# Kernel tuning notes

Hardware: AMD Instinct MI355X
Metric: run time of the kernel (lower is better)

## Reference

```python
import jax, jax.numpy as jnp
import numpy as np
from jax import lax

B, L = 4, 1024
D_MODEL = 512
D_INNER = 2 * D_MODEL            # expand=2 -> 1024
HEADDIM = 64
NHEADS = D_INNER // HEADDIM      # 16
D_STATE = 64
D_CONV = 4
NLAYERS = 2
NTOKEN = 60695
PAD_IDX = 60694
NCLS = 164
CONV_DIM = D_INNER + 2 * D_STATE            # 1152 (ngroups=1)
D_IN_PROJ = 2 * D_INNER + 2 * D_STATE + NHEADS  # 2192
MAX_VALUE = 512.0
EPS = 1e-5


def _ln(x, g=None, b=None):
    m = jnp.mean(x, -1, keepdims=True)
    v = jnp.mean((x - m) ** 2, -1, keepdims=True)
    y = (x - m) * lax.rsqrt(v + EPS)
    return y if g is None else y * g + b


def _smart_flip(X, pad_mask):
    # reverse only the valid (non-pad) prefix of each sequence
    lengths = (~pad_mask).sum(1)
    rng = jnp.arange(X.shape[1])[None, :]
    flip = rng < lengths[:, None]
    pos = jnp.where(flip, lengths[:, None] - 1 - rng, rng)
    return jnp.take_along_axis(X, pos[:, :, None], axis=1)


def _mamba2(u, in_w, conv_w, conv_b, A_log, dt_bias, Dskip, norm_w, out_w):
    # Mamba2 block (mamba_ssm defaults: ngroups=1, silu conv act, gated RMSNorm)
    Bb, Ll, _ = u.shape
    zxbcdt = u @ in_w.T                                      # (B,L,D_IN_PROJ)
    z = zxbcdt[..., :D_INNER]
    xBC = zxbcdt[..., D_INNER:D_INNER + CONV_DIM]
    dt = jax.nn.softplus(zxbcdt[..., -NHEADS:] + dt_bias)    # (B,L,H)
    # causal depthwise conv1d + silu
    xBC = jnp.pad(xBC, ((0, 0), (D_CONV - 1, 0), (0, 0))).transpose(0, 2, 1)
    xBC = lax.conv_general_dilated(xBC, conv_w[:, None, :], (1,), 'VALID',
                                   feature_group_count=CONV_DIM)
    xBC = jax.nn.silu(xBC.transpose(0, 2, 1) + conv_b)       # (B,L,CONV_DIM)
    x = xBC[..., :D_INNER].reshape(Bb, Ll, NHEADS, HEADDIM)
    Bm = xBC[..., D_INNER:D_INNER + D_STATE]                 # (B,L,N)
    Cm = xBC[..., D_INNER + D_STATE:]                        # (B,L,N)
    dA = jnp.exp(dt * (-jnp.exp(A_log)))                     # (B,L,H)

    def step(h, t):
        dA_t, dt_t, x_t, B_t, C_t = t
        # h: (B,H,P,N)
        h = h * dA_t[:, :, None, None] \
            + (dt_t[:, :, None] * x_t)[..., None] * B_t[:, None, None, :]
        y = jnp.einsum('bhpn,bn->bhp', h, C_t)
        return h, y

    h0 = jnp.zeros((Bb, NHEADS, HEADDIM, D_STATE), u.dtype)
    xs = (dA.transpose(1, 0, 2), dt.transpose(1, 0, 2),
          x.transpose(1, 0, 2, 3), Bm.transpose(1, 0, 2), Cm.transpose(1, 0, 2))
    _, ys = lax.scan(step, h0, xs)                            # (L,B,H,P)
    y = ys.transpose(1, 0, 2, 3) + Dskip[None, None, :, None] * x
    y = y.reshape(Bb, Ll, D_INNER)
    y = y * jax.nn.silu(z)                                    # gated RMSNorm
    y = y * lax.rsqrt(jnp.mean(y * y, -1, keepdims=True) + EPS) * norm_w
    return y @ out_w.T


def _forward(src, values, pad_mask, embed, ge_ln_g, ge_ln_b,
             ve_w1, ve_b1, ve_w2, ve_b2, ve_ln_g, ve_ln_b,
             in_proj_w, conv_w_f, conv_b_f, A_log_f, dt_bias_f, D_f, norm_w_f,
             conv_w_r, conv_b_r, A_log_r, dt_bias_r, D_r, norm_w_r, out_proj_w,
             expr_w1, expr_b1, expr_w2, expr_b2, expr_w3, expr_b3,
             cls_w1, cls_b1, cls_ln1_g, cls_ln1_b, cls_w2, cls_b2,
             cls_ln2_g, cls_ln2_b, cls_wo, cls_bo):
    src_emb = _ln(embed[src], ge_ln_g, ge_ln_b)
    v = jnp.minimum(values, MAX_VALUE)[..., None]
    v = jax.nn.relu(v @ ve_w1.T + ve_b1)
    v = _ln(v @ ve_w2.T + ve_b2, ve_ln_g, ve_ln_b)
    h = (src_emb + v) * (~pad_mask)[..., None]
    for i in range(NLAYERS):
        hn = _ln(h)  # F.layer_norm without affine
        out = _mamba2(hn, in_proj_w[i], conv_w_f[i], conv_b_f[i], A_log_f[i],
                      dt_bias_f[i], D_f[i], norm_w_f[i], out_proj_w[i])
        rev = _smart_flip(hn, pad_mask)
        out_r = _mamba2(rev, in_proj_w[i], conv_w_r[i], conv_b_r[i], A_log_r[i],
                        dt_bias_r[i], D_r[i], norm_w_r[i], out_proj_w[i])
        out_r = _smart_flip(out_r, pad_mask)
        h = _ln((out + out_r) / 2)
    # ExprDecoder (MLM head)
    e = jax.nn.leaky_relu(h @ expr_w1.T + expr_b1)
    e = jax.nn.leaky_relu(e @ expr_w2.T + expr_b2)
    mlm = (e @ expr_w3.T + expr_b3)[..., 0]
    # cell embedding: cls token
    cell = h[:, 0, :]
    # ClsDecoder
    c = _ln(jax.nn.relu(cell @ cls_w1.T + cls_b1), cls_ln1_g, cls_ln1_b)
    c = _ln(jax.nn.relu(c @ cls_w2.T + cls_b2), cls_ln2_g, cls_ln2_b)
    cls = c @ cls_wo.T + cls_bo
    return mlm, cell, cls


def setup_inputs() -> dict:
    key = jax.random.key(0)
    ks = iter(jax.random.split(key, 64))
    w = lambda *s: jax.random.normal(next(ks), s, jnp.float32) * 0.02
    embed = w(NTOKEN, D_MODEL).at[PAD_IDX].set(0.0)
    dt_u = jax.random.uniform(next(ks), (NLAYERS, NHEADS), minval=1e-3, maxval=0.1)
    dt_u2 = jax.random.uniform(next(ks), (NLAYERS, NHEADS), minval=1e-3, maxval=0.1)
    return dict(
        src=jax.random.randint(next(ks), (B, L), 0, PAD_IDX),
        values=jax.random.uniform(next(ks), (B, L), jnp.float32),
        src_key_padding_mask=jnp.zeros((B, L), bool),
        embed=embed,
        ge_ln_g=jnp.ones((D_MODEL,)), ge_ln_b=jnp.zeros((D_MODEL,)),
        ve_w1=w(D_MODEL, 1), ve_b1=jnp.zeros((D_MODEL,)),
        ve_w2=w(D_MODEL, D_MODEL), ve_b2=jnp.zeros((D_MODEL,)),
        ve_ln_g=jnp.ones((D_MODEL,)), ve_ln_b=jnp.zeros((D_MODEL,)),
        in_proj_w=w(NLAYERS, D_IN_PROJ, D_MODEL),
        conv_w_f=w(NLAYERS, CONV_DIM, D_CONV), conv_b_f=jnp.zeros((NLAYERS, CONV_DIM)),
        A_log_f=jnp.log(jax.random.uniform(next(ks), (NLAYERS, NHEADS), minval=1.0, maxval=16.0)),
        dt_bias_f=dt_u + jnp.log(-jnp.expm1(-dt_u)),
        D_f=jnp.ones((NLAYERS, NHEADS)), norm_w_f=jnp.ones((NLAYERS, D_INNER)),
        conv_w_r=w(NLAYERS, CONV_DIM, D_CONV), conv_b_r=jnp.zeros((NLAYERS, CONV_DIM)),
        A_log_r=jnp.log(jax.random.uniform(next(ks), (NLAYERS, NHEADS), minval=1.0, maxval=16.0)),
        dt_bias_r=dt_u2 + jnp.log(-jnp.expm1(-dt_u2)),
        D_r=jnp.ones((NLAYERS, NHEADS)), norm_w_r=jnp.ones((NLAYERS, D_INNER)),
        out_proj_w=w(NLAYERS, D_MODEL, D_INNER),
        expr_w1=w(D_MODEL, D_MODEL), expr_b1=jnp.zeros((D_MODEL,)),
        expr_w2=w(D_MODEL, D_MODEL), expr_b2=jnp.zeros((D_MODEL,)),
        expr_w3=w(1, D_MODEL), expr_b3=jnp.zeros((1,)),
        cls_w1=w(D_MODEL, D_MODEL), cls_b1=jnp.zeros((D_MODEL,)),
        cls_ln1_g=jnp.ones((D_MODEL,)), cls_ln1_b=jnp.zeros((D_MODEL,)),
        cls_w2=w(D_MODEL, D_MODEL), cls_b2=jnp.zeros((D_MODEL,)),
        cls_ln2_g=jnp.ones((D_MODEL,)), cls_ln2_b=jnp.zeros((D_MODEL,)),
        cls_wo=w(NCLS, D_MODEL), cls_bo=jnp.zeros((NCLS,)),
    )


def reference(src, values, src_key_padding_mask, embed, ge_ln_g, ge_ln_b,
              ve_w1, ve_b1, ve_w2, ve_b2, ve_ln_g, ve_ln_b,
              in_proj_w, conv_w_f, conv_b_f, A_log_f, dt_bias_f, D_f, norm_w_f,
              conv_w_r, conv_b_r, A_log_r, dt_bias_r, D_r, norm_w_r, out_proj_w,
              expr_w1, expr_b1, expr_w2, expr_b2, expr_w3, expr_b3,
              cls_w1, cls_b1, cls_ln1_g, cls_ln1_b, cls_w2, cls_b2,
              cls_ln2_g, cls_ln2_b, cls_wo, cls_bo):
    return _forward(src, values, src_key_padding_mask, embed, ge_ln_g, ge_ln_b,
                    ve_w1, ve_b1, ve_w2, ve_b2, ve_ln_g, ve_ln_b,
                    in_proj_w, conv_w_f, conv_b_f, A_log_f, dt_bias_f, D_f, norm_w_f,
                    conv_w_r, conv_b_r, A_log_r, dt_bias_r, D_r, norm_w_r, out_proj_w,
                    expr_w1, expr_b1, expr_w2, expr_b2, expr_w3, expr_b3,
                    cls_w1, cls_b1, cls_ln1_g, cls_ln1_b, cls_w2, cls_b2,
                    cls_ln2_g, cls_ln2_b, cls_wo, cls_bo)
```

## Files before the change

kernel.cpp:

```cpp
#include <hip/hip_runtime.h>
#include <hip/hip_bf16.h>
#include <math.h>

constexpr int Bb = 4, Ls = 1024, DM = 512, DI = 1024, NH = 16, HD = 64, DS = 64;
constexpr int CDIM = DI + 2 * DS;
constexpr int DIP  = 2 * DI + 2 * DS + NH;
constexpr int NPJ  = 2 * DI + 2 * DS;
constexpr float EPSf = 1e-5f;
constexpr int TOK = Bb * Ls;
constexpr int CH = 64, NCH = Ls / CH;

#define DEVI __device__ __forceinline__

using bfrag = __attribute__((ext_vector_type(8))) short;
using f4v   = __attribute__((ext_vector_type(4))) float;
using u16x8 = __attribute__((ext_vector_type(8))) unsigned short;

#define GLOAD16(gp, lp)                                                              \
  __builtin_amdgcn_global_load_lds((__attribute__((address_space(1))) void*)(gp),   \
                                   (__attribute__((address_space(3))) void*)(lp),   \
                                   16, 0, 0)

DEVI float wsum(float v) {
#pragma unroll
  for (int o = 32; o > 0; o >>= 1) v += __shfl_xor(v, o);
  return v;
}
DEVI float sigmoidf_(float x) { return 1.f / (1.f + __expf(-x)); }
DEVI unsigned short f2bf(float x) {
  union { float f; unsigned u; } c{x};
  unsigned u = c.u;
  u += 0x7fffu + ((u >> 16) & 1u);
  return (unsigned short)(u >> 16);
}
DEVI float bf2f(unsigned short u) {
  union { unsigned u; float f; } c{(unsigned)u << 16};
  return c.f;
}

DEVI void ld8(const float* __restrict__ p, int lane, float (&x)[8]) {
  float4 a = *(const float4*)(p + lane * 4);
  float4 b = *(const float4*)(p + 256 + lane * 4);
  x[0] = a.x; x[1] = a.y; x[2] = a.z; x[3] = a.w;
  x[4] = b.x; x[5] = b.y; x[6] = b.z; x[7] = b.w;
}
DEVI void ld8bf(const unsigned short* __restrict__ p, int lane, float (&x)[8]) {
  ushort4 a = *(const ushort4*)(p + lane * 4);
  ushort4 b = *(const ushort4*)(p + 256 + lane * 4);
  x[0] = bf2f(a.x); x[1] = bf2f(a.y); x[2] = bf2f(a.z); x[3] = bf2f(a.w);
  x[4] = bf2f(b.x); x[5] = bf2f(b.y); x[6] = bf2f(b.z); x[7] = bf2f(b.w);
}
DEVI void st8(float* __restrict__ p, int lane, const float (&x)[8]) {
  *(float4*)(p + lane * 4) = make_float4(x[0], x[1], x[2], x[3]);
  *(float4*)(p + 256 + lane * 4) = make_float4(x[4], x[5], x[6], x[7]);
}
DEVI void st8bf(unsigned short* __restrict__ p, int lane, const float (&x)[8]) {
  *(ushort4*)(p + lane * 4) = make_ushort4(f2bf(x[0]), f2bf(x[1]), f2bf(x[2]), f2bf(x[3]));
  *(ushort4*)(p + 256 + lane * 4) = make_ushort4(f2bf(x[4]), f2bf(x[5]), f2bf(x[6]), f2bf(x[7]));
}
DEVI void norm8(float (&x)[8]) {
  float s = 0;
#pragma unroll
  for (int j = 0; j < 8; ++j) s += x[j];
  float mean = wsum(s) * (1.f / 512.f);
#pragma unroll
  for (int j = 0; j < 8; ++j) x[j] -= mean;
  float q = 0;
#pragma unroll
  for (int j = 0; j < 8; ++j) q += x[j] * x[j];
  float var = wsum(q) * (1.f / 512.f);
  float inv = rsqrtf(var + EPSf);
#pragma unroll
  for (int j = 0; j < 8; ++j) x[j] *= inv;
}

__global__ __launch_bounds__(256) void k_w2bf(const float* __restrict__ in,
                                              unsigned short* __restrict__ out, int n8) {
  int i = blockIdx.x * 256 + threadIdx.x;
  if (i >= n8) return;
  const float4* p = (const float4*)in + (size_t)i * 2;
  float4 a = p[0], b = p[1];
  *((ushort4*)out + (size_t)i * 2) = make_ushort4(f2bf(a.x), f2bf(a.y), f2bf(a.z), f2bf(a.w));
  *((ushort4*)out + (size_t)i * 2 + 1) = make_ushort4(f2bf(b.x), f2bf(b.y), f2bf(b.z), f2bf(b.w));
}

__global__ __launch_bounds__(256) void k_embed(const int* __restrict__ src, const float* __restrict__ values,
    const float* __restrict__ embed, const float* __restrict__ gg, const float* __restrict__ gb,
    const float* __restrict__ vw1, const float* __restrict__ vb1,
    float* __restrict__ hbuf, unsigned short* __restrict__ v1bf) {
  int gw = (blockIdx.x * 256 + threadIdx.x) >> 6;
  int lane = threadIdx.x & 63;
  if (gw >= TOK) return;
  const float* er = embed + (size_t)src[gw] * DM;
  float x[8];
  ld8(er, lane, x);
  norm8(x);
  float g[8], bv[8];
  ld8(gg, lane, g); ld8(gb, lane, bv);
#pragma unroll
  for (int j = 0; j < 8; ++j) x[j] = x[j] * g[j] + bv[j];
  st8(hbuf + (size_t)gw * DM, lane, x);
  float val = fminf(values[gw], 512.f);
  float w1[8], b1[8];
  ld8(vw1, lane, w1); ld8(vb1, lane, b1);
  float v[8];
#pragma unroll
  for (int j = 0; j < 8; ++j) v[j] = fmaxf(val * w1[j] + b1[j], 0.f);
  st8bf(v1bf + (size_t)gw * DM, lane, v);
}

__global__ __launch_bounds__(256) void k_haddv(const float* __restrict__ t2, const float* __restrict__ g,
    const float* __restrict__ bb, const unsigned char* __restrict__ mask, float* __restrict__ hbuf) {
  int gw = (blockIdx.x * 256 + threadIdx.x) >> 6;
  int lane = threadIdx.x & 63;
  if (gw >= TOK) return;
  float x[8];
  ld8(t2 + (size_t)gw * DM, lane, x);
  norm8(x);
  float gv[8], bv[8], h[8];
  ld8(g, lane, gv); ld8(bb, lane, bv);
  ld8(hbuf + (size_t)gw * DM, lane, h);
  float mf = mask[gw] ? 0.f : 1.f;
#pragma unroll
  for (int j = 0; j < 8; ++j) h[j] = (h[j] + x[j] * gv[j] + bv[j]) * mf;
  st8(hbuf + (size_t)gw * DM, lane, h);
}

__global__ __launch_bounds__(256) void k_lndt(const float* __restrict__ pre, const float* __restrict__ inw,
    const float* __restrict__ dtbF, const float* __restrict__ AlogF,
    const float* __restrict__ dtbR, const float* __restrict__ AlogR,
    const int* __restrict__ len, unsigned short* __restrict__ hnbf,
    float* __restrict__ dtf, float* __restrict__ laf,
    float* __restrict__ dtr, float* __restrict__ lar) {
  int gw = (blockIdx.x * 256 + threadIdx.x) >> 6;
  int lane = threadIdx.x & 63;
  if (gw >= TOK) return;
  float x[8];
  ld8(pre + (size_t)gw * DM, lane, x);
  norm8(x);
  st8bf(hnbf + (size_t)gw * DM, lane, x);
  const float* wdt = inw + (size_t)NPJ * DM;
  float myraw = 0.f;
#pragma unroll
  for (int hh = 0; hh < NH; ++hh) {
    float w[8];
    ld8(wdt + (size_t)hh * DM, lane, w);
    float s = 0;
#pragma unroll
    for (int j = 0; j < 8; ++j) s += x[j] * w[j];
    s = wsum(s);
    if (lane == hh) myraw = s;
  }
  if (lane < NH) {
    int t = gw & (Ls - 1), b = gw >> 10;
    int ln = len[b];
    int pos = (t < ln) ? (ln - 1 - t) : t;
    size_t grev = (size_t)(b * Ls + pos);
    float rf = myraw + dtbF[lane];
    float df = rf > 20.f ? rf : log1pf(__expf(rf));
    dtf[(size_t)gw * NH + lane] = df;
    laf[(size_t)gw * NH + lane] = -__expf(AlogF[lane]) * df;
    float rr = myraw + dtbR[lane];
    float dr = rr > 20.f ? rr : log1pf(__expf(rr));
    dtr[grev * NH + lane] = dr;
    lar[grev * NH + lane] = -__expf(AlogR[lane]) * dr;
  }
}

template <int ACT, int OMODE>
__global__ __launch_bounds__(256) void gemm_bf(const unsigned short* __restrict__ A,
    const unsigned short* __restrict__ W, const float* __restrict__ bias,
    void* __restrict__ Cout, int M, int N, int K) {
  constexpr int BK = 64;
  __shared__ unsigned short As[128 * BK];
  __shared__ unsigned short Bs[128 * BK];
  int tid = threadIdx.x;
  int bm = blockIdx.y * 128, bn = blockIdx.x * 128;
  int wv = tid >> 6, lane = tid & 63;
  int mb = (wv >> 1) * 64, nb = (wv & 1) * 64;
  int rA = lane >> 3;
  int cswz = (lane & 7) ^ rA;
  f4v acc[4][4] = {};

  for (int k0 = 0; k0 < K; k0 += BK) {
#pragma unroll
    for (int q = 0; q < 4; ++q) {
      int ch = wv * 4 + q;
      const unsigned short* ga = A + (size_t)(bm + ch * 8 + rA) * K + k0 + cswz * 8;
      GLOAD16(ga, &As[ch * 512]);
      const unsigned short* gb = W + (size_t)(bn + ch * 8 + rA) * K + k0 + cswz * 8;
      GLOAD16(gb, &Bs[ch * 512]);
    }
    __syncthreads();
#pragma unroll
    for (int ks = 0; ks < BK; ks += 32) {
      int kb = (ks >> 3) + (lane >> 4);
      bfrag af[4], bg[4];
#pragma unroll
      for (int i = 0; i < 4; ++i) {
        int ra_ = mb + i * 16 + (lane & 15);
        af[i] = *(const bfrag*)((const char*)As + ((ra_ * 128 + kb * 16) ^ ((ra_ & 7) << 4)));
        int rb_ = nb + i * 16 + (lane & 15);
        bg[i] = *(const bfrag*)((const char*)Bs + ((rb_ * 128 + kb * 16) ^ ((rb_ & 7) << 4)));
      }
#pragma unroll
      for (int i = 0; i < 4; ++i)
#pragma unroll
        for (int j = 0; j < 4; ++j)
          acc[i][j] = __builtin_amdgcn_mfma_f32_16x16x32_bf16(af[i], bg[j], acc[i][j], 0, 0, 0);
    }
    __syncthreads();
  }

  int cb = bn + nb + (lane & 15);
  int rb = bm + mb + ((lane >> 4) << 2);
#pragma unroll
  for (int j = 0; j < 4; ++j) {
    float bv = bias ? bias[cb + j * 16] : 0.f;
#pragma unroll
    for (int i = 0; i < 4; ++i) {
#pragma unroll
      for (int r = 0; r < 4; ++r) {
        float v = acc[i][j][r] + bv;
        if (ACT == 1) v = fmaxf(v, 0.f);
        if (ACT == 2) v = v > 0.f ? v : 0.01f * v;
        size_t idx = (size_t)(rb + i * 16 + r) * N + cb + j * 16;
        if (OMODE == 0) ((float*)Cout)[idx] = v;
        else ((unsigned short*)Cout)[idx] = f2bf(v);
      }
    }
  }
}

__global__ __launch_bounds__(256) void k_convbc(const unsigned short* __restrict__ zx,
    const float* __restrict__ cwF, const float* __restrict__ cbF,
    const float* __restrict__ cwR, const float* __restrict__ cbR,
    const int* __restrict__ len, unsigned short* __restrict__ bcbuf) {
  int idx = blockIdx.x * 256 + threadIdx.x;
  if (idx >= 2 * TOK * 128) return;
  int col = idx & 127;
  int bt = (idx >> 7) & (TOK - 1);
  int dir = idx >> 19;
  int b = bt >> 10, t = bt & (Ls - 1);
  int ln = len[b];
  const float* cw = dir ? cwR : cwF;
  const float* cb = dir ? cbR : cbF;
  int ccd = DI + col;
  float4 w4 = *(const float4*)(cw + ccd * 4);
  float s = cb[ccd];
  float wk[4] = {w4.x, w4.y, w4.z, w4.w};
#pragma unroll
  for (int k = 0; k < 4; ++k) {
    int rl = t - 3 + k;
    if (rl >= 0) {
      int gr = dir ? (rl < ln ? ln - 1 - rl : rl) : rl;
      s += wk[k] * bf2f(zx[((size_t)(b * Ls + gr)) * NPJ + 2 * DI + col]);
    }
  }
  s = s * sigmoidf_(s);
  bcbuf[idx] = f2bf(s);
}

__global__ __launch_bounds__(256) void k_chunk(const unsigned short* __restrict__ zx,
    const unsigned short* __restrict__ bcbuf,
    const float* __restrict__ cwF, const float* __restrict__ cbF,
    const float* __restrict__ cwR, const float* __restrict__ cbR,
    const float* __restrict__ dtF, const float* __restrict__ laF,
    const float* __restrict__ dtR, const float* __restrict__ laR,
    const float* __restrict__ DkF, const float* __restrict__ DkR,
    const int* __restrict__ len,
    unsigned short* __restrict__ yF, unsigned short* __restrict__ yR,
    unsigned short* __restrict__ gbuf, float* __restrict__ cumbuf) {
  __shared__ unsigned short Cb[4096], Bbs[4096], BbT[4096], xT[4096], Wt[4096];
  __shared__ float ldsL[64], sdt_[64], fs[64];
  int blk2 = blockIdx.x;
  int dir = blk2 >> 10;
  int blk = blk2 & 1023;
  int c = blk & 15, bh = blk >> 4, h = bh & 15, b = bh >> 4;
  int tid = threadIdx.x, wv = tid >> 6, lane = tid & 63;
  int c0 = c * CH;
  int ln = len[b];
  const float* cw = dir ? cwR : cwF;
  const float* cbias = dir ? cbR : cbF;
  const float* dtp = dir ? dtR : dtF;
  const float* ldap = dir ? laR : laF;
  float Dh = (dir ? DkR : DkF)[h];
  unsigned short* y = dir ? yR : yF;

  if (tid < 64) {
    size_t off = ((size_t)(b * Ls + c0 + tid)) * NH + h;
    float dtv = dtp[off];
    float v = ldap[off];
#pragma unroll
    for (int o = 1; o < 64; o <<= 1) {
      float n = __shfl_up(v, o);
      if (tid >= o) v += n;
    }
    ldsL[tid] = v;
    sdt_[tid] = dtv;
    cumbuf[(size_t)blk2 * 64 + tid] = __expf(v);
    float L63 = __shfl(v, 63);
    fs[tid] = __expf(L63 - v) * dtv;
  }
  __syncthreads();

  {
    const unsigned short* bc = bcbuf + ((size_t)(dir * TOK + b * Ls + c0)) * 128;
    int r = tid >> 2;
    int colq = (tid & 3) * 32;
#pragma unroll
    for (int g = 0; g < 2; ++g) {
      int col = colq + g * 16;
      u16x8 v0 = *(const u16x8*)(bc + (size_t)r * 128 + col);
      u16x8 v1 = *(const u16x8*)(bc + (size_t)r * 128 + col + 8);
      if (col < 64) {
        *(u16x8*)((char*)Bbs + ((r * 128 + col * 2) ^ ((r & 7) << 4))) = v0;
        *(u16x8*)((char*)Bbs + ((r * 128 + col * 2 + 16) ^ ((r & 7) << 4))) = v1;
      } else {
        int n = col - 64;
        *(u16x8*)((char*)Cb + ((r * 128 + n * 2) ^ ((r & 7) << 4))) = v0;
        *(u16x8*)((char*)Cb + ((r * 128 + n * 2 + 16) ^ ((r & 7) << 4))) = v1;
      }
    }
  }
  {
    int n = tid & 63;
    int tg = (tid >> 6) * 16;
    const unsigned short* bc = bcbuf + ((size_t)(dir * TOK + b * Ls + c0 + tg)) * 128 + n;
    float vals[16];
#pragma unroll
    for (int t = 0; t < 16; ++t) vals[t] = bf2f(bc[(size_t)t * 128]) * fs[tg + t];
#pragma unroll
    for (int hv = 0; hv < 2; ++hv) {
      u16x8 pk;
#pragma unroll
      for (int k = 0; k < 8; ++k) pk[k] = f2bf(vals[hv * 8 + k]);
      *(u16x8*)((char*)BbT + ((n * 128 + (tg + hv * 8) * 2) ^ ((n & 7) << 4))) = pk;
    }
  }
  {
    int cch = tid & 63;
    int tg = (tid >> 6) * 16;
    int gcol = DI + h * 64 + cch;
    int ccd = h * 64 + cch;
    float4 w4 = *(const float4*)(cw + ccd * 4);
    float bias = cbias[ccd];
    float vv[19];
#pragma unroll
    for (int k = 0; k < 19; ++k) {
      int rl = c0 + tg - 3 + k;
      float val = 0.f;
      if (rl >= 0) {
        int gr = dir ? (rl < ln ? ln - 1 - rl : rl) : rl;
        val = bf2f(zx[((size_t)(b * Ls + gr)) * NPJ + gcol]);
      }
      vv[k] = val;
    }
    int p = cch;
#pragma unroll
    for (int hv = 0; hv < 2; ++hv) {
      u16x8 pk;
#pragma unroll
      for (int k = 0; k < 8; ++k) {
        int t = hv * 8 + k;
        float s = bias + w4.x * vv[t] + w4.y * vv[t + 1] + w4.z * vv[t + 2] + w4.w * vv[t + 3];
        pk[k] = f2bf(s * sigmoidf_(s));
      }
      *(u16x8*)((char*)xT + ((p * 128 + (tg + hv * 8) * 2) ^ ((p & 7) << 4))) = pk;
    }
  }
  __syncthreads();

  f4v accS[4] = {};
#pragma unroll
  for (int ks = 0; ks < 64; ks += 32) {
    int kb = (ks >> 3) + (lane >> 4);
    int ra = wv * 16 + (lane & 15);
    bfrag af = *(const bfrag*)((const char*)Cb + ((ra * 128 + kb * 16) ^ ((ra & 7) << 4)));
#pragma unroll
    for (int j = 0; j < 4; ++j) {
      int rb = j * 16 + (lane & 15);
      bfrag bg = *(const bfrag*)((const char*)Bbs + ((rb * 128 + kb * 16) ^ ((rb & 7) << 4)));
      accS[j] = __builtin_amdgcn_mfma_f32_16x16x32_bf16(af, bg, accS[j], 0, 0, 0);
    }
  }
  {
    int trow = wv * 16 + ((lane >> 4) << 2);
#pragma unroll
    for (int j = 0; j < 4; ++j) {
      int s = j * 16 + (lane & 15);
      float ds = sdt_[s], Lsv = ldsL[s];
#pragma unroll
      for (int r = 0; r < 4; ++r) {
        int tt = trow + r;
        float wval = (s <= tt) ? accS[j][r] * ds * __expf(ldsL[tt] - Lsv) : 0.f;
        *(unsigned short*)((char*)Wt + ((tt * 128 + s * 2) ^ ((tt & 7) << 4))) = f2bf(wval);
      }
    }
  }
  __syncthreads();

  f4v accY[4] = {}, accG[4] = {};
#pragma unroll
  for (int ks = 0; ks < 64; ks += 32) {
    int kb = (ks >> 3) + (lane >> 4);
    int ra = wv * 16 + (lane & 15);
    bfrag afW = *(const bfrag*)((const char*)Wt + ((ra * 128 + kb * 16) ^ ((ra & 7) << 4)));
    bfrag afB = *(const bfrag*)((const char*)BbT + ((ra * 128 + kb * 16) ^ ((ra & 7) << 4)));
#pragma unroll
    for (int j = 0; j < 4; ++j) {
      int rb = j * 16 + (lane & 15);
      bfrag bg = *(const bfrag*)((const char*)xT + ((rb * 128 + kb * 16) ^ ((rb & 7) << 4)));
      accY[j] = __builtin_amdgcn_mfma_f32_16x16x32_bf16(afW, bg, accY[j], 0, 0, 0);
      accG[j] = __builtin_amdgcn_mfma_f32_16x16x32_bf16(afB, bg, accG[j], 0, 0, 0);
    }
  }
  int trow = wv * 16 + ((lane >> 4) << 2);
#pragma unroll
  for (int j = 0; j < 4; ++j) {
    int p = j * 16 + (lane & 15);
#pragma unroll
    for (int r = 0; r < 4; ++r) {
      int t = trow + r;
      float xval = bf2f(*(const unsigned short*)((const char*)xT + ((p * 128 + t * 2) ^ ((p & 7) << 4))));
      y[((size_t)(b * Ls + c0 + t)) * DI + h * 64 + p] = f2bf(accY[j][r] + Dh * xval);
      gbuf[((size_t)blk2 * 64 + t) * 64 + p] = f2bf(accG[j][r]);
    }
  }
}

__global__ __launch_bounds__(256) void k_chain(unsigned short* __restrict__ gbuf,
                                               const float* __restrict__ cumbuf) {
  int bh = blockIdx.x;
  int tid = threadIdx.x;
  size_t base = (size_t)bh * NCH * 4096 + (size_t)tid * 16;
  float hv[16] = {};
  u16x8 ga = *(const u16x8*)(gbuf + base);
  u16x8 gb_ = *(const u16x8*)(gbuf + base + 8);
  float Pc = cumbuf[(size_t)bh * NCH * 64 + 63];
  for (int c = 0; c < NCH; ++c) {
    u16x8 na = {}, nb = {};
    float Pn = 0.f;
    if (c + 1 < NCH) {
      Pn = cumbuf[((size_t)bh * NCH + c + 1) * 64 + 63];
      na = *(const u16x8*)(gbuf + base + (size_t)(c + 1) * 4096);
      nb = *(const u16x8*)(gbuf + base + (size_t)(c + 1) * 4096 + 8);
    }
    u16x8 oa, ob;
#pragma unroll
    for (int k = 0; k < 8; ++k) { oa[k] = f2bf(hv[k]); ob[k] = f2bf(hv[8 + k]); }
    *(u16x8*)(gbuf + base + (size_t)c * 4096) = oa;
    *(u16x8*)(gbuf + base + (size_t)c * 4096 + 8) = ob;
#pragma unroll
    for (int k = 0; k < 8; ++k) {
      hv[k] = fmaf(Pc, hv[k], bf2f(ga[k]));
      hv[8 + k] = fmaf(Pc, hv[8 + k], bf2f(gb_[k]));
    }
    ga = na; gb_ = nb;
    Pc = Pn;
  }
}

__global__ __launch_bounds__(256) void k_corr(const unsigned short* __restrict__ bcbuf,
    const unsigned short* __restrict__ gbuf, const float* __restrict__ cumbuf,
    unsigned short* __restrict__ yF, unsigned short* __restrict__ yR) {
  int blk2 = blockIdx.x;
  int c = blk2 & 15;
  if (c == 0) return;
  __shared__ unsigned short Ct[4096], HT[4096];
  __shared__ float cdl[64];
  int dir = blk2 >> 10;
  int bh = (blk2 & 1023) >> 4, h = bh & 15, b = bh >> 4;
  int tid = threadIdx.x, wv = tid >> 6, lane = tid & 63;
  int c0 = c * CH;
  unsigned short* y = dir ? yR : yF;
  {
    int r = tid >> 2;
    int colq = (tid & 3) * 16;
    const unsigned short* bc = bcbuf + ((size_t)(dir * TOK + b * Ls + c0 + r)) * 128 + 64 + colq;
    u16x8 v0 = *(const u16x8*)bc;
    u16x8 v1 = *(const u16x8*)(bc + 8);
    *(u16x8*)((char*)Ct + ((r * 128 + colq * 2) ^ ((r & 7) << 4))) = v0;
    *(u16x8*)((char*)Ct + ((r * 128 + colq * 2 + 16) ^ ((r & 7) << 4))) = v1;
  }
  {
    int n = tid >> 2, p0 = (tid & 3) * 16;
    const unsigned short* hr = gbuf + (size_t)blk2 * 4096 + (size_t)n * 64 + p0;
    u16x8 v0 = *(const u16x8*)hr;
    u16x8 v1 = *(const u16x8*)(hr + 8);
#pragma unroll
    for (int k = 0; k < 8; ++k) {
      int p = p0 + k;
      *(unsigned short*)((char*)HT + ((p * 128 + n * 2) ^ ((p & 7) << 4))) = v0[k];
      int p2 = p0 + 8 + k;
      *(unsigned short*)((char*)HT + ((p2 * 128 + n * 2) ^ ((p2 & 7) << 4))) = v1[k];
    }
  }
  if (tid < 64) cdl[tid] = cumbuf[(size_t)blk2 * 64 + tid];
  __syncthreads();

  f4v acc[4] = {};
#pragma unroll
  for (int ks = 0; ks < 64; ks += 32) {
    int kb = (ks >> 3) + (lane >> 4);
    int ra = wv * 16 + (lane & 15);
    bfrag af = *(const bfrag*)((const char*)Ct + ((ra * 128 + kb * 16) ^ ((ra & 7) << 4)));
#pragma unroll
    for (int j = 0; j < 4; ++j) {
      int rb = j * 16 + (lane & 15);
      bfrag bg = *(const bfrag*)((const char*)HT + ((rb * 128 + kb * 16) ^ ((rb & 7) << 4)));
      acc[j] = __builtin_amdgcn_mfma_f32_16x16x32_bf16(af, bg, acc[j], 0, 0, 0);
    }
  }
  int trow = wv * 16 + ((lane >> 4) << 2);
#pragma unroll
  for (int j = 0; j < 4; ++j) {
    int p = j * 16 + (lane & 15);
#pragma unroll
    for (int r = 0; r < 4; ++r) {
      int t = trow + r;
      unsigned short* yp = &y[((size_t)(b * Ls + c0 + t)) * DI + h * 64 + p];
      *yp = f2bf(bf2f(*yp) + cdl[t] * acc[j][r]);
    }
  }
}

__global__ __launch_bounds__(256) void k_gab(const unsigned short* __restrict__ yF,
    const unsigned short* __restrict__ yR, const unsigned short* __restrict__ zxb,
    const float* __restrict__ nwF, const float* __restrict__ nwR,
    const int* __restrict__ len, unsigned short* __restrict__ ybf) {
  int w = (blockIdx.x * 256 + threadIdx.x) >> 6;
  int lane = threadIdx.x & 63;
  if (w >= TOK) return;
  int t = w & (Ls - 1), b = w >> 10;
  int ln = len[b];
  int r = b * Ls + ((t < ln) ? (ln - 1 - t) : t);
  const unsigned short* yf = yF + (size_t)w * DI;
  const unsigned short* yr = yR + (size_t)r * DI;
  const unsigned short* zr = zxb + (size_t)w * NPJ;
  float gf[16], gr[16];
  float ssf = 0.f, ssr = 0.f;
#pragma unroll
  for (int q = 0; q < 4; ++q) {
    ushort4 yv = *(const ushort4*)(yf + lane * 4 + q * 256);
    ushort4 rv = *(const ushort4*)(yr + lane * 4 + q * 256);
    ushort4 zu = *(const ushort4*)(zr + lane * 4 + q * 256);
    float z0 = bf2f(zu.x), z1 = bf2f(zu.y), z2 = bf2f(zu.z), z3 = bf2f(zu.w);
    float s0 = z0 * sigmoidf_(z0), s1 = z1 * sigmoidf_(z1), s2 = z2 * sigmoidf_(z2), s3 = z3 * sigmoidf_(z3);
    gf[4 * q + 0] = bf2f(yv.x) * s0; gf[4 * q + 1] = bf2f(yv.y) * s1;
    gf[4 * q + 2] = bf2f(yv.z) * s2; gf[4 * q + 3] = bf2f(yv.w) * s3;
    gr[4 * q + 0] = bf2f(rv.x) * s0; gr[4 * q + 1] = bf2f(rv.y) * s1;
    gr[4 * q + 2] = bf2f(rv.z) * s2; gr[4 * q + 3] = bf2f(rv.w) * s3;
#pragma unroll
    for (int j = 0; j < 4; ++j) {
      ssf += gf[4 * q + j] * gf[4 * q + j];
      ssr += gr[4 * q + j] * gr[4 * q + j];
    }
  }
  ssf = wsum(ssf);
  ssr = wsum(ssr);
  float scf = 0.5f * rsqrtf(ssf * (1.f / (float)DI) + EPSf);
  float scr = 0.5f * rsqrtf(ssr * (1.f / (float)DI) + EPSf);
#pragma unroll
  for (int q = 0; q < 4; ++q) {
    float4 nf = *(const float4*)(nwF + lane * 4 + q * 256);
    float4 nr = *(const float4*)(nwR + lane * 4 + q * 256);
    float o0 = gf[4 * q + 0] * scf * nf.x + gr[4 * q + 0] * scr * nr.x;
    float o1 = gf[4 * q + 1] * scf * nf.y + gr[4 * q + 1] * scr * nr.y;
    float o2 = gf[4 * q + 2] * scf * nf.z + gr[4 * q + 2] * scr * nr.z;
    float o3 = gf[4 * q + 3] * scf * nf.w + gr[4 * q + 3] * scr * nr.w;
    *(ushort4*)(ybf + (size_t)w * DI + lane * 4 + q * 256) =
        make_ushort4(f2bf(o0), f2bf(o1), f2bf(o2), f2bf(o3));
  }
}

__global__ __launch_bounds__(256) void k_hl2(const float* __restrict__ src,
                                             unsigned short* __restrict__ dstbf) {
  int gw = (blockIdx.x * 256 + threadIdx.x) >> 6;
  int lane = threadIdx.x & 63;
  if (gw >= TOK) return;
  float x[8];
  ld8(src + (size_t)gw * DM, lane, x);
  norm8(x);
  st8bf(dstbf + (size_t)gw * DM, lane, x);
}

__global__ __launch_bounds__(256) void k_lengths(const unsigned char* __restrict__ mask, int* __restrict__ len) {
  int b = blockIdx.x;
  int tid = threadIdx.x;
  int cnt = 0;
  for (int t = tid; t < Ls; t += 256) cnt += mask[b * Ls + t] ? 0 : 1;
#pragma unroll
  for (int o = 32; o > 0; o >>= 1) cnt += __shfl_xor(cnt, o);
  __shared__ int red[4];
  if ((tid & 63) == 0) red[tid >> 6] = cnt;
  __syncthreads();
  if (tid == 0) len[b] = red[0] + red[1] + red[2] + red[3];
}

__global__ __launch_bounds__(256) void k_mlm(const unsigned short* __restrict__ e2,
                                             const float* __restrict__ w3,
                                             const float* __restrict__ b3, float* __restrict__ out) {
  int gw = (blockIdx.x * 256 + threadIdx.x) >> 6;
  int lane = threadIdx.x & 63;
  if (gw >= TOK) return;
  float x[8], w[8];
  ld8bf(e2 + (size_t)gw * DM, lane, x);
  ld8(w3, lane, w);
  float s = 0;
#pragma unroll
  for (int j = 0; j < 8; ++j) s += x[j] * w[j];
  s = wsum(s);
  if (lane == 0) out[gw] = s + b3[0];
}

__global__ __launch_bounds__(256) void k_cell(const float* __restrict__ onew, float* __restrict__ out,
                                              float* __restrict__ cc0) {
  int b = threadIdx.x >> 6;
  int lane = threadIdx.x & 63;
  float x[8];
  ld8(onew + (size_t)b * Ls * DM, lane, x);
  norm8(x);
  st8(out + (size_t)b * DM, lane, x);
  st8(cc0 + (size_t)b * DM, lane, x);
}

__global__ __launch_bounds__(256) void k_clsmv(const float* __restrict__ xin, size_t xstride,
    const float* __restrict__ g, const float* __restrict__ bb, int doLN,
    const float* __restrict__ W, const float* __restrict__ bias, int doRelu,
    float* __restrict__ out, int nout) {
  int b = blockIdx.y;
  int j = blockIdx.x * 4 + (threadIdx.x >> 6);
  int lane = threadIdx.x & 63;
  if (j >= nout) return;
  float x[8];
  ld8(xin + (size_t)b * xstride, lane, x);
  if (doLN) {
    norm8(x);
    float gv[8], bv[8];
    ld8(g, lane, gv); ld8(bb, lane, bv);
#pragma unroll
    for (int k = 0; k < 8; ++k) x[k] = x[k] * gv[k] + bv[k];
  }
  float w[8];
  ld8(W + (size_t)j * DM, lane, w);
  float s = 0;
#pragma unroll
  for (int k = 0; k < 8; ++k) s += x[k] * w[k];
  s = wsum(s);
  if (lane == 0) {
    float v = s + bias[j];
    if (doRelu) v = fmaxf(v, 0.f);
    out[(size_t)b * nout + j] = v;
  }
}

constexpr size_t F_H   = 0;
constexpr size_t F_DTF = F_H + (size_t)TOK * DM;
constexpr size_t F_LAF = F_DTF + (size_t)TOK * NH;
constexpr size_t F_DTR = F_LAF + (size_t)TOK * NH;
constexpr size_t F_LAR = F_DTR + (size_t)TOK * NH;
constexpr size_t F_ON  = F_LAR + (size_t)TOK * NH;
constexpr size_t F_CUM = F_ON + (size_t)TOK * DM;
constexpr size_t F_CC0 = F_CUM + (size_t)2 * Bb * NH * NCH * 64;
constexpr size_t F_CC1 = F_CC0 + Bb * DM;
constexpr size_t F_CC2 = F_CC1 + Bb * DM;
constexpr size_t F_LEN = F_CC2 + Bb * DM;
constexpr size_t F_END = F_LEN + 16;
constexpr size_t U0     = F_END * 2;
constexpr size_t UW_IN  = U0;
constexpr size_t UW_OUT = UW_IN + (size_t)2 * DIP * DM;
constexpr size_t UW_VE  = UW_OUT + (size_t)2 * DM * DI;
constexpr size_t UW_E1  = UW_VE + (size_t)DM * DM;
constexpr size_t UW_E2  = UW_E1 + (size_t)DM * DM;
constexpr size_t U_BFA  = UW_E2 + (size_t)DM * DM;
constexpr size_t U_HNBF = U_BFA + (size_t)TOK * DM;
constexpr size_t U_YBF  = U_HNBF + (size_t)TOK * DM;
constexpr size_t U_ZX   = U_YBF + (size_t)TOK * DI;
constexpr size_t U_YF   = U_ZX + (size_t)TOK * NPJ;
constexpr size_t U_YR   = U_YF + (size_t)TOK * DI;
constexpr size_t U_G    = U_YR + (size_t)TOK * DI;

extern "C" void kernel_launch(void* const* d_in, const int* in_sizes, int n_in,
                              void* d_out, int out_size, void* d_ws, size_t ws_size,
                              hipStream_t stream) {
  const int* src = (const int*)d_in[0];
  const float* values = (const float*)d_in[1];
  const unsigned char* mask = (const unsigned char*)d_in[2];
  const float* embed = (const float*)d_in[3];
  const float* ge_g = (const float*)d_in[4];
  const float* ge_b = (const float*)d_in[5];
  const float* ve_w1 = (const float*)d_in[6];
  const float* ve_b1 = (const float*)d_in[7];
  const float* ve_w2 = (const float*)d_in[8];
  const float* ve_b2 = (const float*)d_in[9];
  const float* ve_g = (const float*)d_in[10];
  const float* ve_bb = (const float*)d_in[11];
  const float* in_w = (const float*)d_in[12];
  const float* conv_w_f = (const float*)d_in[13];
  const float* conv_b_f = (const float*)d_in[14];
  const float* A_f = (const float*)d_in[15];
  const float* dtb_f = (const float*)d_in[16];
  const float* D_f = (const float*)d_in[17];
  const float* nw_f = (const float*)d_in[18];
  const float* conv_w_r = (const float*)d_in[19];
  const float* conv_b_r = (const float*)d_in[20];
  const float* A_r = (const float*)d_in[21];
  const float* dtb_r = (const float*)d_in[22];
  const float* D_r = (const float*)d_in[23];
  const float* nw_r = (const float*)d_in[24];
  const float* out_w = (const float*)d_in[25];
  const float* expr_w1 = (const float*)d_in[26];
  const float* expr_b1 = (const float*)d_in[27];
  const float* expr_w2 = (const float*)d_in[28];
  const float* expr_b2 = (const float*)d_in[29];
  const float* expr_w3 = (const float*)d_in[30];
  const float* expr_b3 = (const float*)d_in[31];
  const float* cls_w1 = (const float*)d_in[32];
  const float* cls_b1 = (const float*)d_in[33];
  const float* cls_g1 = (const float*)d_in[34];
  const float* cls_bb1 = (const float*)d_in[35];
  const float* cls_w2 = (const float*)d_in[36];
  const float* cls_b2 = (const float*)d_in[37];
  const float* cls_g2 = (const float*)d_in[38];
  const float* cls_bb2 = (const float*)d_in[39];
  const float* cls_wo = (const float*)d_in[40];
  const float* cls_bo = (const float*)d_in[41];

  float* ws = (float*)d_ws;
  unsigned short* wsu = (unsigned short*)d_ws;
  float* h = ws + F_H;
  float* dtf = ws + F_DTF;
  float* laf = ws + F_LAF;
  float* dtr = ws + F_DTR;
  float* lar = ws + F_LAR;
  float* onew = ws + F_ON;
  float* cumb = ws + F_CUM;
  float* cc0 = ws + F_CC0;
  float* cc1 = ws + F_CC1;
  float* cc2 = ws + F_CC2;
  int* len = (int*)(ws + F_LEN);
  unsigned short* w_in = wsu + UW_IN;
  unsigned short* w_out = wsu + UW_OUT;
  unsigned short* w_ve = wsu + UW_VE;
  unsigned short* w_e1 = wsu + UW_E1;
  unsigned short* w_e2 = wsu + UW_E2;
  unsigned short* bfa = wsu + U_BFA;
  unsigned short* hnbf = wsu + U_HNBF;
  unsigned short* ybf = wsu + U_YBF;
  unsigned short* zxb = wsu + U_ZX;
  unsigned short* yFb = wsu + U_YF;
  unsigned short* yRb = wsu + U_YR;
  unsigned short* gbuf = wsu + U_G;
  unsigned short* bcbuf = ybf;
  float* t2 = onew;
  unsigned short* e2b = zxb;
  float* out = (float*)d_out;

  {
    int n;
    n = 2 * DIP * DM / 8;  k_w2bf<<<(n + 255) / 256, 256, 0, stream>>>(in_w, w_in, n);
    n = 2 * DM * DI / 8;   k_w2bf<<<(n + 255) / 256, 256, 0, stream>>>(out_w, w_out, n);
    n = DM * DM / 8;       k_w2bf<<<(n + 255) / 256, 256, 0, stream>>>(ve_w2, w_ve, n);
    n = DM * DM / 8;       k_w2bf<<<(n + 255) / 256, 256, 0, stream>>>(expr_w1, w_e1, n);
    n = DM * DM / 8;       k_w2bf<<<(n + 255) / 256, 256, 0, stream>>>(expr_w2, w_e2, n);
  }

  k_embed<<<TOK / 4, 256, 0, stream>>>(src, values, embed, ge_g, ge_b, ve_w1, ve_b1, h, bfa);
  gemm_bf<0, 0><<<dim3(DM / 128, TOK / 128), 256, 0, stream>>>(bfa, w_ve, ve_b2, t2, TOK, DM, DM);
  k_haddv<<<TOK / 4, 256, 0, stream>>>(t2, ve_g, ve_bb, mask, h);
  k_lengths<<<Bb, 256, 0, stream>>>(mask, len);

  for (int i = 0; i < 2; ++i) {
    const float* inw = in_w + (size_t)i * DIP * DM;
    unsigned short* inwb = w_in + (size_t)i * DIP * DM;
    unsigned short* outwb = w_out + (size_t)i * DM * DI;
    const float* cwF = conv_w_f + (size_t)i * CDIM * 4;
    const float* cbF = conv_b_f + (size_t)i * CDIM;
    const float* cwR = conv_w_r + (size_t)i * CDIM * 4;
    const float* cbR = conv_b_r + (size_t)i * CDIM;
    const float* pre = (i == 0) ? h : onew;
    k_lndt<<<TOK / 4, 256, 0, stream>>>(pre, inw, dtb_f + i * NH, A_f + i * NH,
                                        dtb_r + i * NH, A_r + i * NH, len, hnbf,
                                        dtf, laf, dtr, lar);
    gemm_bf<0, 1><<<dim3(NPJ / 128, TOK / 128), 256, 0, stream>>>(hnbf, inwb, nullptr, zxb, TOK, NPJ, DM);
    k_convbc<<<(2 * TOK * 128) / 256, 256, 0, stream>>>(zxb, cwF, cbF, cwR, cbR, len, bcbuf);
    k_chunk<<<2 * Bb * NH * NCH, 256, 0, stream>>>(zxb, bcbuf, cwF, cbF, cwR, cbR,
        dtf, laf, dtr, lar, D_f + i * NH, D_r + i * NH, len, yFb, yRb, gbuf, cumb);
    k_chain<<<2 * Bb * NH, 256, 0, stream>>>(gbuf, cumb);
    k_corr<<<2 * Bb * NH * NCH, 256, 0, stream>>>(bcbuf, gbuf, cumb, yFb, yRb);
    k_gab<<<TOK / 4, 256, 0, stream>>>(yFb, yRb, zxb, nw_f + (size_t)i * DI, nw_r + (size_t)i * DI,
                                       len, ybf);
    gemm_bf<0, 0><<<dim3(DM / 128, TOK / 128), 256, 0, stream>>>(ybf, outwb, nullptr, onew, TOK, DM, DI);
  }

  k_hl2<<<TOK / 4, 256, 0, stream>>>(onew, hnbf);
  gemm_bf<2, 1><<<dim3(DM / 128, TOK / 128), 256, 0, stream>>>(hnbf, w_e1, expr_b1, bfa, TOK, DM, DM);
  gemm_bf<2, 1><<<dim3(DM / 128, TOK / 128), 256, 0, stream>>>(bfa, w_e2, expr_b2, e2b, TOK, DM, DM);
  k_mlm<<<TOK / 4, 256, 0, stream>>>(e2b, expr_w3, expr_b3, out);
  k_cell<<<1, 256, 0, stream>>>(onew, out + TOK, cc0);
  k_clsmv<<<dim3(128, Bb), 256, 0, stream>>>(cc0, DM, nullptr, nullptr, 0,
                                             cls_w1, cls_b1, 1, cc1, DM);
  k_clsmv<<<dim3(128, Bb), 256, 0, stream>>>(cc1, DM, cls_g1, cls_bb1, 1,
                                             cls_w2, cls_b2, 1, cc2, DM);
  k_clsmv<<<dim3(41, Bb), 256, 0, stream>>>(cc2, DM, cls_g2, cls_bb2, 1,
                                            cls_wo, cls_bo, 0, out + TOK + Bb * DM, 164);
}
```

Baseline: 322.2 us.

## Merge weight casts, stage dt weights in LDS, split chain scan, fold cell norm

The five weight-conversion launches become one kernel. k_lndt now stages the 16 dt-projection rows (32 KB) in shared memory per block. k_chunk builds the transposed scaled B tile from LDS instead of reloading it from global memory. k_chain runs on twice as many blocks with 8 elements per thread and prefetches two chunks ahead, and the cell-token layernorm moves into k_hl2 so k_cell is removed. The 32 KB LDS per block in k_lndt may reduce occupancy and adds a preload cost to every block.

```diff
diff --git a/kernel.cpp b/kernel.cpp
--- a/kernel.cpp
+++ b/kernel.cpp
@@ -74,14 +74,28 @@
   for (int j = 0; j < 8; ++j) x[j] *= inv;
 }
 
-__global__ __launch_bounds__(256) void k_w2bf(const float* __restrict__ in,
-                                              unsigned short* __restrict__ out, int n8) {
-  int i = blockIdx.x * 256 + threadIdx.x;
-  if (i >= n8) return;
+DEVI void cvt8(const float* __restrict__ in, unsigned short* __restrict__ out, int i) {
   const float4* p = (const float4*)in + (size_t)i * 2;
   float4 a = p[0], b = p[1];
   *((ushort4*)out + (size_t)i * 2) = make_ushort4(f2bf(a.x), f2bf(a.y), f2bf(a.z), f2bf(a.w));
   *((ushort4*)out + (size_t)i * 2 + 1) = make_ushort4(f2bf(b.x), f2bf(b.y), f2bf(b.z), f2bf(b.w));
+}
+__global__ __launch_bounds__(256) void k_w2bf5(
+    const float* __restrict__ s0, unsigned short* __restrict__ d0, int n0,
+    const float* __restrict__ s1, unsigned short* __restrict__ d1, int n1,
+    const float* __restrict__ s2, unsigned short* __restrict__ d2, int n2,
+    const float* __restrict__ s3, unsigned short* __restrict__ d3, int n3,
+    const float* __restrict__ s4, unsigned short* __restrict__ d4, int n4) {
+  int i = blockIdx.x * 256 + threadIdx.x;
+  if (i < n0) { cvt8(s0, d0, i); return; }
+  i -= n0;
+  if (i < n1) { cvt8(s1, d1, i); return; }
+  i -= n1;
+  if (i < n2) { cvt8(s2, d2, i); return; }
+  i -= n2;
+  if (i < n3) { cvt8(s3, d3, i); return; }
+  i -= n3;
+  if (i < n4) { cvt8(s4, d4, i); return; }
 }
 
 __global__ __launch_bounds__(256) void k_embed(const int* __restrict__ src, const float* __restrict__ values,
@@ -132,6 +146,12 @@
     const int* __restrict__ len, unsigned short* __restrict__ hnbf,
     float* __restrict__ dtf, float* __restrict__ laf,
     float* __restrict__ dtr, float* __restrict__ lar) {
+  __shared__ float wdts[NH * DM];
+  {
+    const float4* src4 = (const float4*)(inw + (size_t)NPJ * DM);
+    for (int i = threadIdx.x; i < NH * DM / 4; i += 256) ((float4*)wdts)[i] = src4[i];
+  }
+  __syncthreads();
   int gw = (blockIdx.x * 256 + threadIdx.x) >> 6;
   int lane = threadIdx.x & 63;
   if (gw >= TOK) return;
@@ -139,12 +159,11 @@
   ld8(pre + (size_t)gw * DM, lane, x);
   norm8(x);
   st8bf(hnbf + (size_t)gw * DM, lane, x);
-  const float* wdt = inw + (size_t)NPJ * DM;
   float myraw = 0.f;
 #pragma unroll
   for (int hh = 0; hh < NH; ++hh) {
     float w[8];
-    ld8(wdt + (size_t)hh * DM, lane, w);
+    ld8(wdts + hh * DM, lane, w);
     float s = 0;
 #pragma unroll
     for (int j = 0; j < 8; ++j) s += x[j] * w[j];
@@ -324,21 +343,6 @@
     }
   }
   {
-    int n = tid & 63;
-    int tg = (tid >> 6) * 16;
-    const unsigned short* bc = bcbuf + ((size_t)(dir * TOK + b * Ls + c0 + tg)) * 128 + n;
-    float vals[16];
-#pragma unroll
-    for (int t = 0; t < 16; ++t) vals[t] = bf2f(bc[(size_t)t * 128]) * fs[tg + t];
-#pragma unroll
-    for (int hv = 0; hv < 2; ++hv) {
-      u16x8 pk;
-#pragma unroll
-      for (int k = 0; k < 8; ++k) pk[k] = f2bf(vals[hv * 8 + k]);
-      *(u16x8*)((char*)BbT + ((n * 128 + (tg + hv * 8) * 2) ^ ((n & 7) << 4))) = pk;
-    }
-  }
-  {
     int cch = tid & 63;
     int tg = (tid >> 6) * 16;
     int gcol = DI + h * 64 + cch;
@@ -385,6 +389,24 @@
     }
   }
   {
+    int n = tid & 63;
+    int tg = (tid >> 6) * 16;
+    float vals[16];
+#pragma unroll
+    for (int t = 0; t < 16; ++t) {
+      int s = tg + t;
+      unsigned short raw = *(const unsigned short*)((const char*)Bbs + ((s * 128 + n * 2) ^ ((s & 7) << 4)));
+      vals[t] = bf2f(raw) * fs[s];
+    }
+#pragma unroll
+    for (int hv = 0; hv < 2; ++hv) {
+      u16x8 pk;
+#pragma unroll
+      for (int k = 0; k < 8; ++k) pk[k] = f2bf(vals[hv * 8 + k]);
+      *(u16x8*)((char*)BbT + ((n * 128 + (tg + hv * 8) * 2) ^ ((n & 7) << 4))) = pk;
+    }
+  }
+  {
     int trow = wv * 16 + ((lane >> 4) << 2);
 #pragma unroll
     for (int j = 0; j < 4; ++j) {
@@ -431,33 +453,28 @@
 
 __global__ __launch_bounds__(256) void k_chain(unsigned short* __restrict__ gbuf,
                                                const float* __restrict__ cumbuf) {
-  int bh = blockIdx.x;
-  int tid = threadIdx.x;
-  size_t base = (size_t)bh * NCH * 4096 + (size_t)tid * 16;
-  float hv[16] = {};
-  u16x8 ga = *(const u16x8*)(gbuf + base);
-  u16x8 gb_ = *(const u16x8*)(gbuf + base + 8);
-  float Pc = cumbuf[(size_t)bh * NCH * 64 + 63];
+  int blk = blockIdx.x;
+  int grp = blk >> 1, sp = blk & 1;
+  size_t base = (size_t)grp * NCH * 4096 + sp * 2048 + (size_t)threadIdx.x * 8;
+  const float* cum = cumbuf + (size_t)grp * NCH * 64 + 63;
+  float hv[8] = {};
+  u16x8 g0 = *(const u16x8*)(gbuf + base);
+  u16x8 g1 = *(const u16x8*)(gbuf + base + 4096);
+  float P0 = cum[0], P1 = cum[64];
   for (int c = 0; c < NCH; ++c) {
-    u16x8 na = {}, nb = {};
-    float Pn = 0.f;
-    if (c + 1 < NCH) {
-      Pn = cumbuf[((size_t)bh * NCH + c + 1) * 64 + 63];
-      na = *(const u16x8*)(gbuf + base + (size_t)(c + 1) * 4096);
-      nb = *(const u16x8*)(gbuf + base + (size_t)(c + 1) * 4096 + 8);
-    }
-    u16x8 oa, ob;
-#pragma unroll
-    for (int k = 0; k < 8; ++k) { oa[k] = f2bf(hv[k]); ob[k] = f2bf(hv[8 + k]); }
-    *(u16x8*)(gbuf + base + (size_t)c * 4096) = oa;
-    *(u16x8*)(gbuf + base + (size_t)c * 4096 + 8) = ob;
-#pragma unroll
-    for (int k = 0; k < 8; ++k) {
-      hv[k] = fmaf(Pc, hv[k], bf2f(ga[k]));
-      hv[8 + k] = fmaf(Pc, hv[8 + k], bf2f(gb_[k]));
-    }
-    ga = na; gb_ = nb;
-    Pc = Pn;
+    u16x8 g2 = {};
+    float P2 = 0.f;
+    if (c + 2 < NCH) {
+      g2 = *(const u16x8*)(gbuf + base + (size_t)(c + 2) * 4096);
+      P2 = cum[(size_t)(c + 2) * 64];
+    }
+    u16x8 o;
+#pragma unroll
+    for (int k = 0; k < 8; ++k) o[k] = f2bf(hv[k]);
+    *(u16x8*)(gbuf + base + (size_t)c * 4096) = o;
+#pragma unroll
+    for (int k = 0; k < 8; ++k) hv[k] = fmaf(P0, hv[k], bf2f(g0[k]));
+    g0 = g1; g1 = g2; P0 = P1; P1 = P2;
   }
 }
 
@@ -575,7 +592,7 @@
 }
 
 __global__ __launch_bounds__(256) void k_hl2(const float* __restrict__ src,
-                                             unsigned short* __restrict__ dstbf) {
+    unsigned short* __restrict__ dstbf, float* __restrict__ cellout, float* __restrict__ cc0) {
   int gw = (blockIdx.x * 256 + threadIdx.x) >> 6;
   int lane = threadIdx.x & 63;
   if (gw >= TOK) return;
@@ -583,6 +600,11 @@
   ld8(src + (size_t)gw * DM, lane, x);
   norm8(x);
   st8bf(dstbf + (size_t)gw * DM, lane, x);
+  if ((gw & (Ls - 1)) == 0) {
+    int b = gw >> 10;
+    st8(cellout + (size_t)b * DM, lane, x);
+    st8(cc0 + (size_t)b * DM, lane, x);
+  }
 }
 
 __global__ __launch_bounds__(256) void k_lengths(const unsigned char* __restrict__ mask, int* __restrict__ len) {
@@ -612,17 +634,6 @@
   for (int j = 0; j < 8; ++j) s += x[j] * w[j];
   s = wsum(s);
   if (lane == 0) out[gw] = s + b3[0];
-}
-
-__global__ __launch_bounds__(256) void k_cell(const float* __restrict__ onew, float* __restrict__ out,
-                                              float* __restrict__ cc0) {
-  int b = threadIdx.x >> 6;
-  int lane = threadIdx.x & 63;
-  float x[8];
-  ld8(onew + (size_t)b * Ls * DM, lane, x);
-  norm8(x);
-  st8(out + (size_t)b * DM, lane, x);
-  st8(cc0 + (size_t)b * DM, lane, x);
 }
 
 __global__ __launch_bounds__(256) void k_clsmv(const float* __restrict__ xin, size_t xstride,
@@ -758,12 +769,11 @@
   float* out = (float*)d_out;
 
   {
-    int n;
-    n = 2 * DIP * DM / 8;  k_w2bf<<<(n + 255) / 256, 256, 0, stream>>>(in_w, w_in, n);
-    n = 2 * DM * DI / 8;   k_w2bf<<<(n + 255) / 256, 256, 0, stream>>>(out_w, w_out, n);
-    n = DM * DM / 8;       k_w2bf<<<(n + 255) / 256, 256, 0, stream>>>(ve_w2, w_ve, n);
-    n = DM * DM / 8;       k_w2bf<<<(n + 255) / 256, 256, 0, stream>>>(expr_w1, w_e1, n);
-    n = DM * DM / 8;       k_w2bf<<<(n + 255) / 256, 256, 0, stream>>>(expr_w2, w_e2, n);
+    int n0 = 2 * DIP * DM / 8, n1 = 2 * DM * DI / 8, n2 = DM * DM / 8, n3 = n2, n4 = n2;
+    int tot = n0 + n1 + n2 + n3 + n4;
+    k_w2bf5<<<(tot + 255) / 256, 256, 0, stream>>>(in_w, w_in, n0, out_w, w_out, n1,
+                                                   ve_w2, w_ve, n2, expr_w1, w_e1, n3,
+                                                   expr_w2, w_e2, n4);
   }
 
   k_embed<<<TOK / 4, 256, 0, stream>>>(src, values, embed, ge_g, ge_b, ve_w1, ve_b1, h, bfa);
@@ -787,18 +797,17 @@
     k_convbc<<<(2 * TOK * 128) / 256, 256, 0, stream>>>(zxb, cwF, cbF, cwR, cbR, len, bcbuf);
     k_chunk<<<2 * Bb * NH * NCH, 256, 0, stream>>>(zxb, bcbuf, cwF, cbF, cwR, cbR,
         dtf, laf, dtr, lar, D_f + i * NH, D_r + i * NH, len, yFb, yRb, gbuf, cumb);
-    k_chain<<<2 * Bb * NH, 256, 0, stream>>>(gbuf, cumb);
+    k_chain<<<2 * 2 * Bb * NH, 256, 0, stream>>>(gbuf, cumb);
     k_corr<<<2 * Bb * NH * NCH, 256, 0, stream>>>(bcbuf, gbuf, cumb, yFb, yRb);
     k_gab<<<TOK / 4, 256, 0, stream>>>(yFb, yRb, zxb, nw_f + (size_t)i * DI, nw_r + (size_t)i * DI,
                                        len, ybf);
     gemm_bf<0, 0><<<dim3(DM / 128, TOK / 128), 256, 0, stream>>>(ybf, outwb, nullptr, onew, TOK, DM, DI);
   }
 
-  k_hl2<<<TOK / 4, 256, 0, stream>>>(onew, hnbf);
+  k_hl2<<<TOK / 4, 256, 0, stream>>>(onew, hnbf, out + TOK, cc0);
   gemm_bf<2, 1><<<dim3(DM / 128, TOK / 128), 256, 0, stream>>>(hnbf, w_e1, expr_b1, bfa, TOK, DM, DM);
   gemm_bf<2, 1><<<dim3(DM / 128, TOK / 128), 256, 0, stream>>>(bfa, w_e2, expr_b2, e2b, TOK, DM, DM);
   k_mlm<<<TOK / 4, 256, 0, stream>>>(e2b, expr_w3, expr_b3, out);
-  k_cell<<<1, 256, 0, stream>>>(onew, out + TOK, cc0);
   k_clsmv<<<dim3(128, Bb), 256, 0, stream>>>(cc0, DM, nullptr, nullptr, 0,
                                              cls_w1, cls_b1, 1, cc1, DM);
   k_clsmv<<<dim3(128, Bb), 256, 0, stream>>>(cc1, DM, cls_g1, cls_bb1, 1,
```

Result: faster. 313.0 us (-2.8%).
